# Optimization experiments

Measured on AMD Instinct MI355X. Metric: run time of the kernel, lower is better.

The kernel has to match this reference:

```python
import jax, jax.numpy as jnp
import numpy as np

B, N, H, R = 128, 512, 256, 3
VIRTUAL_DECAY = 0.7


def _build_tree():
    # Deterministic random recursive tree: parent[i] ~ U[0, i)
    rng = np.random.default_rng(0)
    parent = np.zeros(N, np.int64)
    for i in range(1, N):
        parent[i] = rng.integers(0, i)
    depth = np.zeros(N, np.int64)
    for i in range(1, N):
        depth[i] = depth[parent[i]] + 1
    rel_edge = rng.integers(0, R, N)          # relation type of edge (parent -> i)
    virtual = rng.random(N) < 0.1
    children = [[] for _ in range(N)]
    for i in range(1, N):
        children[parent[i]].append(i)
    # Group internal nodes by depth (deepest first == valid post-order batching),
    # pad ragged child lists per level.
    levels = []
    for d in range(int(depth.max()), -1, -1):
        nodes = [n for n in range(N) if depth[n] == d and len(children[n]) > 0]
        if not nodes:
            continue
        cmax = max(len(children[n]) for n in nodes)
        M = len(nodes)
        cidx = np.zeros((M, cmax), np.int64)
        cmask = np.zeros((M, cmax), np.float32)
        crel = np.zeros((M, cmax), np.int64)
        cvirt = np.zeros((M, cmax), bool)
        for m, n in enumerate(nodes):
            ch = children[n]
            k = len(ch)
            cidx[m, :k] = ch
            cmask[m, :k] = 1.0
            crel[m, :k] = rel_edge[ch]
            cvirt[m, :k] = virtual[ch]
        levels.append((jnp.array(nodes), jnp.array(cidx), jnp.array(cmask),
                       jnp.array(crel), jnp.array(cvirt)))
    return levels

LEVELS = _build_tree()


def _forward(node_features, W_enc, b_enc, rel_emb, W_i, b_i, W_o, b_o, W_u, b_u,
             W_f, b_f, w_attn, b_attn):
    h = node_features @ W_enc + b_enc            # (B, N, H) node_encoder
    c = jnp.zeros_like(h)
    for node_ids, cidx, cmask, crel, cvirt in LEVELS:
        x = h[:, node_ids]                       # (B, M, H) input_vec (== encoded feats)
        ch_h = h[:, cidx]                        # (B, M, C, H)
        ch_c = c[:, cidx]
        # virtual-node decay + padding mask
        decay = jnp.where(cvirt, VIRTUAL_DECAY, 1.0).astype(h.dtype) * cmask  # (M, C)
        ch_h = ch_h * decay[None, :, :, None]
        ch_c = ch_c * decay[None, :, :, None]
        # relation-aware attention over children
        re = rel_emb[crel]                       # (M, C, H)
        scores = jnp.einsum('bmch,h->bmc', re[None] + ch_h, w_attn) + b_attn[0]
        scores = jnp.where(cmask[None] > 0, scores, -1e9)
        attw = jax.nn.softmax(scores, axis=-1)   # (B, M, C)
        h_sum = jnp.einsum('bmc,bmch->bmh', attw, ch_h)
        # per-relation forget transform (note: original applies NO sigmoid here)
        f = jnp.zeros_like(ch_h)
        for r in range(R):
            fr = jnp.einsum('bmch,hk->bmck', ch_h, W_f[r]) + b_f[r]
            f = f + fr * (crel == r).astype(h.dtype)[None, :, :, None]
        c_sum = jnp.sum(f * ch_c, axis=2)        # (B, M, H); padded ch_c is 0
        comb = jnp.concatenate([x, h_sum], axis=-1)  # (B, M, 2H)
        i_g = jax.nn.sigmoid(comb @ W_i + b_i)
        o_g = jax.nn.sigmoid(comb @ W_o + b_o)
        u_g = jnp.tanh(comb @ W_u + b_u)
        c_new = i_g * u_g + c_sum
        h_new = o_g * jnp.tanh(c_new)
        h = h.at[:, node_ids].set(h_new)
        c = c.at[:, node_ids].set(c_new)
    return h[:, 0]                               # pooling == 'root' (root = 0)


def setup_inputs() -> dict:
    key = jax.random.key(0)
    ks = jax.random.split(key, 8)
    s = 0.05
    f32 = jnp.float32
    return {
        'node_features': jax.random.normal(ks[0], (B, N, H), f32),
        'W_enc': jax.random.normal(ks[1], (H, H), f32) * s,
        'b_enc': jnp.full((H,), 0.1, f32),
        'rel_emb': jax.random.normal(ks[2], (R, H), f32) * s,
        'W_i': jax.random.normal(ks[3], (2 * H, H), f32) * s,
        'b_i': jnp.full((H,), 0.1, f32),
        'W_o': jax.random.normal(ks[4], (2 * H, H), f32) * s,
        'b_o': jnp.full((H,), 0.1, f32),
        'W_u': jax.random.normal(ks[5], (2 * H, H), f32) * s,
        'b_u': jnp.full((H,), 0.1, f32),
        'W_f': jax.random.normal(ks[6], (R, H, H), f32) * s,
        'b_f': jnp.full((R, H), 0.1, f32),
        'w_attn': jax.random.normal(ks[7], (H,), f32) * s,
        'b_attn': jnp.full((1,), 0.1, f32),
    }


def reference(node_features, W_enc, b_enc, rel_emb, W_i, b_i, W_o, b_o, W_u, b_u,
              W_f, b_f, w_attn, b_attn):
    return _forward(node_features, W_enc, b_enc, rel_emb, W_i, b_i, W_o, b_o,
                    W_u, b_u, W_f, b_f, w_attn, b_attn)
```

## Files before the change

### kernel.cpp

```cpp
#include <hip/hip_runtime.h>
#include <stdint.h>
#include <string.h>
#include <math.h>

#define NB 128
#define NN 512
#define NH 256
#define NR 3

typedef __attribute__((ext_vector_type(8))) short bh8;
typedef __attribute__((ext_vector_type(4))) float f32x4;

struct Pcg {
  __uint128_t state, inc;
  bool has32; uint32_t buf32;
};

static const __uint128_t PCG_MULT =
    (((__uint128_t)2549297995355413924ULL) << 64) | 4865540595714422341ULL;

static inline uint64_t pcg_next64(Pcg& s) {
  s.state = s.state * PCG_MULT + s.inc;
  uint64_t hi = (uint64_t)(s.state >> 64), lo = (uint64_t)s.state;
  uint64_t x = hi ^ lo;
  unsigned rot = (unsigned)(s.state >> 122) & 63u;
  return (x >> rot) | (x << ((64u - rot) & 63u));
}
static inline uint32_t pcg_next32(Pcg& s) {
  if (s.has32) { s.has32 = false; return s.buf32; }
  uint64_t n = pcg_next64(s);
  s.has32 = true; s.buf32 = (uint32_t)(n >> 32);
  return (uint32_t)n;
}
static inline uint64_t pcg_bounded(Pcg& s, uint64_t high) {
  uint64_t rng = high - 1;
  if (rng == 0) return 0;
  uint32_t rng_excl = (uint32_t)rng + 1u;
  uint64_t m = (uint64_t)pcg_next32(s) * (uint64_t)rng_excl;
  uint32_t leftover = (uint32_t)m;
  if (leftover < rng_excl) {
    uint32_t threshold = (uint32_t)((0xFFFFFFFFu - (uint32_t)rng) % rng_excl);
    while (leftover < threshold) {
      m = (uint64_t)pcg_next32(s) * (uint64_t)rng_excl;
      leftover = (uint32_t)m;
    }
  }
  return m >> 32;
}
static inline double pcg_double(Pcg& s) {
  return (double)(pcg_next64(s) >> 11) * (1.0 / 9007199254740992.0);
}

static void pcg_seed0(Pcg& s) {
  uint32_t pool[4];
  uint32_t hc = 0x43b0d7e5u;
  auto hashmix = [&hc](uint32_t v) -> uint32_t {
    v ^= hc; hc *= 0x931e8875u; v *= hc; v ^= v >> 16; return v;
  };
  auto mix = [](uint32_t x, uint32_t y) -> uint32_t {
    uint32_t r = 0xca01f9ddu * x - 0x4973f715u * y; r ^= r >> 16; return r;
  };
  for (int i = 0; i < 4; i++) pool[i] = hashmix(0u);
  for (int src = 0; src < 4; src++)
    for (int dst = 0; dst < 4; dst++)
      if (src != dst) pool[dst] = mix(pool[dst], hashmix(pool[src]));
  uint32_t gs[8]; uint32_t hb = 0x8b51f9ddu;
  for (int i = 0; i < 8; i++) {
    uint32_t dv = pool[i & 3];
    dv ^= hb; hb *= 0x58f38dedu; dv *= hb; dv ^= dv >> 16;
    gs[i] = dv;
  }
  uint64_t w0 = (uint64_t)gs[0] | ((uint64_t)gs[1] << 32);
  uint64_t w1 = (uint64_t)gs[2] | ((uint64_t)gs[3] << 32);
  uint64_t w2 = (uint64_t)gs[4] | ((uint64_t)gs[5] << 32);
  uint64_t w3 = (uint64_t)gs[6] | ((uint64_t)gs[7] << 32);
  __uint128_t initstate = (((__uint128_t)w0) << 64) | w1;
  __uint128_t initseq   = (((__uint128_t)w2) << 64) | w3;
  s.state = 0;
  s.inc = (initseq << 1) | 1;
  s.state = s.state * PCG_MULT + s.inc;
  s.state += initstate;
  s.state = s.state * PCG_MULT + s.inc;
  s.has32 = false; s.buf32 = 0;
}

struct TreeMeta {
  int nodes[512];
  int cstart[512];
  int ccount[512];
  int echild[512];
  int erel[512];
  float edecay[512];
  int cechild[512];
  int cerel[512];
  float cedec[512];
  int cens[513];
};
struct HostTree {
  TreeMeta meta;
  int n_levels;
  int level_off[520];
  int level_M[520];
};

static void build_tree_host(HostTree& T) {
  Pcg st; pcg_seed0(st);
  int parent[NN], depth[NN], rel[NN];
  unsigned char virt[NN];
  parent[0] = 0; depth[0] = 0;
  for (int i = 1; i < NN; i++) parent[i] = (int)pcg_bounded(st, (uint64_t)i);
  for (int i = 1; i < NN; i++) depth[i] = depth[parent[i]] + 1;
  for (int i = 0; i < NN; i++) rel[i] = (int)pcg_bounded(st, (uint64_t)NR);
  for (int i = 0; i < NN; i++) virt[i] = (pcg_double(st) < 0.1) ? 1 : 0;

  int childcnt[NN]; memset(childcnt, 0, sizeof(childcnt));
  for (int i = 1; i < NN; i++) childcnt[parent[i]]++;
  int maxd = 0;
  for (int i = 0; i < NN; i++) if (depth[i] > maxd) maxd = depth[i];

  int ni = 0, ne = 0, nec = 0;
  T.n_levels = 0;
  for (int d = maxd; d >= 0; d--) {
    int mstart = ni;
    for (int n = 0; n < NN; n++) {
      if (depth[n] == d && childcnt[n] > 0) {
        T.meta.nodes[ni] = n;
        T.meta.cstart[ni] = ne;
        T.meta.ccount[ni] = childcnt[n];
        T.meta.cens[ni] = nec;
        for (int i2 = 1; i2 < NN; i2++) {
          if (parent[i2] == n) {
            T.meta.echild[ne] = i2;
            T.meta.erel[ne] = rel[i2];
            T.meta.edecay[ne] = virt[i2] ? 0.7f : 1.0f;
            ne++;
            if (childcnt[i2] > 0) {
              T.meta.cechild[nec] = i2;
              T.meta.cerel[nec] = rel[i2];
              T.meta.cedec[nec] = virt[i2] ? 0.7f : 1.0f;
              nec++;
            }
          }
        }
        ni++;
      }
    }
    if (ni > mstart) {
      T.level_off[T.n_levels] = mstart;
      T.level_M[T.n_levels] = ni - mstart;
      T.n_levels++;
    }
  }
  T.meta.cens[ni] = nec;
}

__device__ __forceinline__ uint16_t f2bf(float f) {
  uint32_t u = __float_as_uint(f);
  return (uint16_t)((u + 0x7fffu + ((u >> 16) & 1u)) >> 16);
}
__device__ __forceinline__ float bf2f(uint16_t b) {
  return __uint_as_float(((uint32_t)b) << 16);
}
__device__ __forceinline__ float sigm(float x) {
  return 1.f / (1.f + expf(-x));
}

__device__ __forceinline__ void stage_bf16(uint16_t* __restrict__ sm,
    const uint16_t* __restrict__ src, int stride, int rows) {
  const int chunks = rows << 3;
  for (int cch = threadIdx.x; cch < chunks; cch += 256) {
    const int row = cch >> 3, k = (cch & 7) << 3;
    uint4 v = *(const uint4*)(src + (size_t)row * stride + k);
    *(uint4*)(sm + (((row << 6) + k) ^ ((row & 7) << 3))) = v;
  }
}
__device__ __forceinline__ void stage_f32(uint16_t* __restrict__ sm,
    const float* __restrict__ src, int stride, int rows) {
  const int chunks = rows << 3;
  for (int cch = threadIdx.x; cch < chunks; cch += 256) {
    const int row = cch >> 3, k = (cch & 7) << 3;
    const float* p = src + (size_t)row * stride + k;
    float4 a = *(const float4*)p, b = *(const float4*)(p + 4);
    uint4 w;
    w.x = (uint32_t)f2bf(a.x) | ((uint32_t)f2bf(a.y) << 16);
    w.y = (uint32_t)f2bf(a.z) | ((uint32_t)f2bf(a.w) << 16);
    w.z = (uint32_t)f2bf(b.x) | ((uint32_t)f2bf(b.y) << 16);
    w.w = (uint32_t)f2bf(b.z) | ((uint32_t)f2bf(b.w) << 16);
    *(uint4*)(sm + (((row << 6) + k) ^ ((row & 7) << 3))) = w;
  }
}
__device__ __forceinline__ bh8 fld(const uint16_t* __restrict__ sm, int row, int k) {
  return *(const bh8*)(sm + (((row << 6) + k) ^ ((row & 7) << 3)));
}

#define LDROW(BUF, CH) do { \
    const uint4* p_ = (const uint4*)(hbase + (size_t)(CH) * NH); \
    BUF[0]=p_[0]; BUF[1]=p_[1]; BUF[2]=p_[2]; BUF[3]=p_[3]; \
    BUF[4]=p_[4]; BUF[5]=p_[5]; BUF[6]=p_[6]; BUF[7]=p_[7]; } while (0)
#define ACCROW(BUF, W) do { const float w_ = (W); \
    _Pragma("unroll") for (int v_ = 0; v_ < 8; v_++) { \
      const uint16_t* pe_ = (const uint16_t*)&BUF[v_]; \
      _Pragma("unroll") for (int q_ = 0; q_ < 8; q_++) \
        hs[v_*8+q_] = fmaf(bf2f(pe_[q_]), w_, hs[v_*8+q_]); } } while (0)

__global__ __launch_bounds__(256) void k_prep(const float* __restrict__ We,
    const float* __restrict__ Wf, const float* __restrict__ Wi,
    const float* __restrict__ Wo, const float* __restrict__ Wu,
    uint16_t* __restrict__ WeT, uint16_t* __restrict__ WfT,
    uint16_t* __restrict__ WgT) {
  const int i = blockIdx.x * 256 + threadIdx.x;
  if (i < 65536) {
    const int n = i >> 8, k = i & 255;
    WeT[i] = f2bf(We[k * 256 + n]);
  }
  const int i2 = i - 65536;
  if (i2 >= 0 && i2 < 196608) {
    const int r = i2 >> 16, rem = i2 & 65535, n = rem >> 8, k = rem & 255;
    WfT[i2] = f2bf(Wf[r * 65536 + k * 256 + n]);
  }
  const int i3 = i - 262144;
  if (i3 >= 0 && i3 < 393216) {
    const int g = i3 >> 17, rem = i3 & 131071, n = rem >> 9, k = rem & 511;
    const float* S = (g == 0) ? Wi : (g == 1) ? Wo : Wu;
    WgT[i3] = f2bf(S[k * 256 + n]);
  }
}

__global__ __launch_bounds__(256) void k_enc(const float* __restrict__ nf,
    const uint16_t* __restrict__ WeT, const float* __restrict__ b_enc,
    uint16_t* __restrict__ h_bf, uint16_t* __restrict__ x_enc) {
  __shared__ __align__(16) uint16_t smA[128 * 64];
  __shared__ __align__(16) uint16_t smB[128 * 64];
  const int bm = blockIdx.x * 128, bn = blockIdx.y * 128;
  const int tid = threadIdx.x, wid = tid >> 6, lane = tid & 63;
  const int wr = wid >> 1, wc2 = wid & 1, lr = lane & 15, lk = (lane >> 4) << 3;
  f32x4 acc[4][4] = {};
  for (int k0 = 0; k0 < 256; k0 += 64) {
    __syncthreads();
    stage_f32(smA, nf + (size_t)bm * NH + k0, NH, 128);
    stage_bf16(smB, WeT + (size_t)bn * 256 + k0, 256, 128);
    __syncthreads();
#pragma unroll
    for (int ks = 0; ks < 2; ks++) {
      bh8 af[4], bfr[4];
#pragma unroll
      for (int i = 0; i < 4; i++) af[i] = fld(smA, wr * 64 + i * 16 + lr, ks * 32 + lk);
#pragma unroll
      for (int j = 0; j < 4; j++) bfr[j] = fld(smB, wc2 * 64 + j * 16 + lr, ks * 32 + lk);
#pragma unroll
      for (int i = 0; i < 4; i++)
#pragma unroll
        for (int j = 0; j < 4; j++)
          acc[i][j] = __builtin_amdgcn_mfma_f32_16x16x32_bf16(af[i], bfr[j], acc[i][j], 0, 0, 0);
    }
  }
#pragma unroll
  for (int i = 0; i < 4; i++) {
#pragma unroll
    for (int j = 0; j < 4; j++) {
      const int col = bn + wc2 * 64 + j * 16 + (lane & 15);
      const float be = b_enc[col];
#pragma unroll
      for (int r = 0; r < 4; r++) {
        const int row = bm + wr * 64 + i * 16 + (lane >> 4) * 4 + r;
        const uint16_t hv = f2bf(acc[i][j][r] + be);
        h_bf[(size_t)row * NH + col] = hv;
        x_enc[(size_t)row * NH + col] = hv;
      }
    }
  }
}

__global__ __launch_bounds__(256) void k_sv0(const uint16_t* __restrict__ h_bf,
    const float* __restrict__ w_attn, float* __restrict__ svp) {
  const int idx = blockIdx.x * 256 + threadIdx.x;
  const int g = idx & 15;
  const size_t row = (size_t)(idx >> 4);
  const uint16_t* hp = h_bf + row * NH + g * 16;
  uint4 p0 = *(const uint4*)hp, p1 = *(const uint4*)(hp + 8);
  const uint16_t* e0 = (const uint16_t*)&p0;
  const uint16_t* e1 = (const uint16_t*)&p1;
  float s = 0.f;
#pragma unroll
  for (int u = 0; u < 8; u++) s = fmaf(bf2f(e0[u]), w_attn[g * 16 + u], s);
#pragma unroll
  for (int u = 0; u < 8; u++) s = fmaf(bf2f(e1[u]), w_attn[g * 16 + 8 + u], s);
  svp[idx] = s;
}

__global__ __launch_bounds__(256) void k_tiny(
    uint16_t* h_bf, float* c, float* __restrict__ svp,
    const uint16_t* __restrict__ x_enc,
    const uint16_t* __restrict__ WfT, const uint16_t* __restrict__ WgT,
    const float* __restrict__ b_f, const float* __restrict__ b_i,
    const float* __restrict__ b_o, const float* __restrict__ b_u,
    const float* __restrict__ rel_emb, const float* __restrict__ w_attn,
    const float* __restrict__ b_attn, float* __restrict__ out,
    const TreeMeta* __restrict__ tm, int nb) {
  __shared__ float sc[64 * 65];
  __shared__ float swa[256];
  __shared__ float sRE[3];
  __shared__ int chl[64]; __shared__ int rll[64]; __shared__ float dcl[64];
  __shared__ __align__(16) uint16_t hsum[4 * 4096];

  const int c0 = blockIdx.x * 16;
  const int mloc = blockIdx.y >> 1, b0 = (blockIdx.y & 1) * 64;
  const int gi = nb + mloc;
  const int nd = tm->nodes[gi], cs = tm->cstart[gi], cc = tm->ccount[gi];
  const int ce0 = tm->cens[gi], nic = tm->cens[gi + 1] - ce0;
  const int tid = threadIdx.x, wid = tid >> 6, lane = tid & 63;
  const int lb = lane & 15, lq = lane >> 4;
  const int colw = c0 + lb;
  const int wrow = b0 + wid * 16;

  if (tid < cc) {
    chl[tid] = tm->echild[cs + tid];
    rll[tid] = tm->erel[cs + tid];
    dcl[tid] = tm->edecay[cs + tid];
  }
  swa[tid] = w_attn[tid];
  if (wid < 3) {
    float p = 0.f;
#pragma unroll
    for (int i = 0; i < 4; i++) p += rel_emb[wid * NH + lane + 64 * i] * w_attn[lane + 64 * i];
#pragma unroll
    for (int off = 32; off; off >>= 1) p += __shfl_down(p, off);
    if (lane == 0) sRE[wid] = p;
  }
  __syncthreads();

  const float ba = b_attn[0];
  if (tid < 64) {
    const float* svpb = svp + (size_t)(b0 + tid) * NN * 16;
    for (int e = 0; e < cc; e++) {
      const float4* p = (const float4*)(svpb + chl[e] * 16);
      float4 a = p[0], b2 = p[1], c2 = p[2], d2 = p[3];
      float s = ((a.x + a.y) + (a.z + a.w)) + ((b2.x + b2.y) + (b2.z + b2.w)) +
                ((c2.x + c2.y) + (c2.z + c2.w)) + ((d2.x + d2.y) + (d2.z + d2.w));
      sc[tid * 65 + e] = sRE[rll[e]] + dcl[e] * s + ba;
    }
    float mx = -1e30f;
    for (int e = 0; e < cc; e++) mx = fmaxf(mx, sc[tid * 65 + e]);
    float ss = 0.f;
    for (int e = 0; e < cc; e++) ss += expf(sc[tid * 65 + e] - mx);
    const float inv = 1.0f / ss;
    for (int e = 0; e < cc; e++) sc[tid * 65 + e] = expf(sc[tid * 65 + e] - mx) * inv * dcl[e];
  }
  __syncthreads();

  const int sb = tid >> 2, sq = tid & 3;
  {
    float hs[64];
#pragma unroll
    for (int v = 0; v < 64; v++) hs[v] = 0.f;
    const uint16_t* hbase = h_bf + (size_t)(b0 + sb) * NN * NH + sq * 64;
    uint4 bufA[8], bufB[8];
    LDROW(bufA, chl[0]);
    int e = 0;
    for (; e + 2 <= cc; e += 2) {
      LDROW(bufB, chl[e + 1]);
      ACCROW(bufA, sc[sb * 65 + e]);
      if (e + 2 < cc) LDROW(bufA, chl[e + 2]);
      ACCROW(bufB, sc[sb * 65 + e + 1]);
    }
    if (e < cc) ACCROW(bufA, sc[sb * 65 + e]);
    uint16_t* sub = hsum + sq * 4096;
#pragma unroll
    for (int v = 0; v < 32; v++) {
      uint32_t pk = (uint32_t)f2bf(hs[2 * v]) | ((uint32_t)f2bf(hs[2 * v + 1]) << 16);
      const int elem = ((sb << 6) + 2 * v) ^ ((sb & 7) << 3);
      *(uint32_t*)(sub + elem) = pk;
    }
  }

  f32x4 csum = {};
#pragma unroll 2
  for (int e = 0; e < nic; e++) {
    const int ch = tm->cechild[ce0 + e];
    const int rel = tm->cerel[ce0 + e];
    const float dec = tm->cedec[ce0 + e];
    const uint16_t* Wr = WfT + (size_t)rel * 65536 + (size_t)colw * 256;
    f32x4 facc = {};
#pragma unroll
    for (int k0 = 0; k0 < 8; k0++) {
      const int kk = k0 * 32 + lq * 8;
      const bh8 af = *(const bh8*)(h_bf + ((size_t)(wrow + lb) * NN + ch) * NH + kk);
      const bh8 bq = *(const bh8*)(Wr + kk);
      facc = __builtin_amdgcn_mfma_f32_16x16x32_bf16(af, bq, facc, 0, 0, 0);
    }
    const float bfv = b_f[rel * NH + colw];
#pragma unroll
    for (int r = 0; r < 4; r++) {
      const int brow = wrow + lq * 4 + r;
      const float cch = c[((size_t)brow * NN + ch) * NH + colw];
      csum[r] += (dec * facc[r] + bfv) * (dec * cch);
    }
  }
  __syncthreads();

  f32x4 ga[3] = {};
#pragma unroll
  for (int k32 = 0; k32 < 16; k32++) {
    const int kk = k32 * 32 + lq * 8;
    bh8 af;
    if (k32 < 8) {
      af = *(const bh8*)(x_enc + ((size_t)(wrow + lb) * NN + nd) * NH + kk);
    } else {
      const int kx = k32 - 8;
      af = fld(hsum + (kx >> 1) * 4096, wid * 16 + lb, (kx & 1) * 32 + lq * 8);
    }
#pragma unroll
    for (int g = 0; g < 3; g++) {
      const bh8 bq = *(const bh8*)(WgT + ((size_t)g << 17) + (size_t)colw * 512 + kk);
      ga[g] = __builtin_amdgcn_mfma_f32_16x16x32_bf16(af, bq, ga[g], 0, 0, 0);
    }
  }

  const float bi_ = b_i[colw], bo_ = b_o[colw], bu_ = b_u[colw];
  const float wac = swa[colw];
#pragma unroll
  for (int r = 0; r < 4; r++) {
    const int brow = wrow + lq * 4 + r;
    const size_t idx = ((size_t)brow * NN + nd) * NH + colw;
    const float ig = sigm(ga[0][r] + bi_);
    const float og = sigm(ga[1][r] + bo_);
    const float ug = tanhf(ga[2][r] + bu_);
    const float cn = fmaf(ig, ug, csum[r]);
    c[idx] = cn;
    const float hn = og * tanhf(cn);
    h_bf[idx] = f2bf(hn);
    if (nd == 0) out[(size_t)brow * NH + colw] = hn;
    float pv = hn * wac;
    pv += __shfl_xor(pv, 1); pv += __shfl_xor(pv, 2);
    pv += __shfl_xor(pv, 4); pv += __shfl_xor(pv, 8);
    if (lb == 0) svp[((size_t)brow * NN + nd) * 16 + (c0 >> 4)] = pv;
  }
}

extern "C" void kernel_launch(void* const* d_in, const int* in_sizes, int n_in,
                              void* d_out, int out_size, void* d_ws, size_t ws_size,
                              hipStream_t stream) {
  (void)in_sizes; (void)n_in; (void)out_size; (void)ws_size;
  const float* nf      = (const float*)d_in[0];
  const float* W_enc   = (const float*)d_in[1];
  const float* b_enc   = (const float*)d_in[2];
  const float* rel_emb = (const float*)d_in[3];
  const float* W_i     = (const float*)d_in[4];
  const float* b_i     = (const float*)d_in[5];
  const float* W_o     = (const float*)d_in[6];
  const float* b_o     = (const float*)d_in[7];
  const float* W_u     = (const float*)d_in[8];
  const float* b_u     = (const float*)d_in[9];
  const float* W_f     = (const float*)d_in[10];
  const float* b_f     = (const float*)d_in[11];
  const float* w_attn  = (const float*)d_in[12];
  const float* b_attn  = (const float*)d_in[13];
  float* out = (float*)d_out;

  static HostTree T;
  build_tree_host(T);

  char* ws = (char*)d_ws;
  const size_t OFF_HBF = 32768;
  const size_t SZ_HBF  = (size_t)NB * NN * NH * 2;
  const size_t OFF_XE  = OFF_HBF + SZ_HBF;
  const size_t OFF_WET = OFF_XE + SZ_HBF;
  const size_t OFF_WFT = OFF_WET + 131072;
  const size_t OFF_WGT = OFF_WFT + 393216;
  const size_t OFF_C   = OFF_WGT + 786432;
  const size_t SZ_C    = (size_t)NB * NN * NH * 4;
  const size_t OFF_SVP = OFF_C + SZ_C;

  TreeMeta* dm = (TreeMeta*)ws;
  uint16_t* h_bf = (uint16_t*)(ws + OFF_HBF);
  uint16_t* x_enc = (uint16_t*)(ws + OFF_XE);
  uint16_t* WeT = (uint16_t*)(ws + OFF_WET);
  uint16_t* WfT = (uint16_t*)(ws + OFF_WFT);
  uint16_t* WgT = (uint16_t*)(ws + OFF_WGT);
  float* c = (float*)(ws + OFF_C);
  float* svp = (float*)(ws + OFF_SVP);

  hipMemcpyAsync(dm, &T.meta, sizeof(TreeMeta), hipMemcpyHostToDevice, stream);

  k_prep<<<2560, 256, 0, stream>>>(W_enc, W_f, W_i, W_o, W_u, WeT, WfT, WgT);
  k_enc<<<dim3((NB * NN) / 128, 2), 256, 0, stream>>>(nf, WeT, b_enc, h_bf, x_enc);
  k_sv0<<<dim3((NB * NN * 16) / 256), 256, 0, stream>>>(h_bf, w_attn, svp);

  for (int l = 0; l < T.n_levels; l++) {
    k_tiny<<<dim3(16, 2 * T.level_M[l]), 256, 0, stream>>>(h_bf, c, svp, x_enc,
        WfT, WgT, b_f, b_i, b_o, b_u, rel_emb, w_attn, b_attn, out, dm,
        T.level_off[l]);
  }
}
```

Measured before the change: 653.6 us.

## Split per-level tree LSTM kernel into attention/forget-cell and gate kernels

The fused per-level kernel is split in two. The first kernel does the attention-weighted child hidden sum, written to a global comb buffer, and the forget-gate cell contributions, which run in separate blocks per internal child edge and use atomicAdd into the parent's pre-zeroed c. The second kernel runs the gate GEMM with 64x64 tiles per block over x_enc and comb, which gives better register reuse of weights. This exposes more parallelism and removes the single block's serial loop over children. In exchange it adds a full memset of c, float atomics, an extra launch per level chunk, and a global round trip for comb.

```diff
diff --git a/kernel.cpp b/kernel.cpp
--- a/kernel.cpp
+++ b/kernel.cpp
@@ -92,6 +92,7 @@
   int erel[512];
   float edecay[512];
   int cechild[512];
+  int cepar[512];
   int cerel[512];
   float cedec[512];
   int cens[513];
@@ -136,6 +137,7 @@
             ne++;
             if (childcnt[i2] > 0) {
               T.meta.cechild[nec] = i2;
+              T.meta.cepar[nec] = n;
               T.meta.cerel[nec] = rel[i2];
               T.meta.cedec[nec] = virt[i2] ? 0.7f : 1.0f;
               nec++;
@@ -288,68 +290,92 @@
   svp[idx] = s;
 }
 
-__global__ __launch_bounds__(256) void k_tiny(
-    uint16_t* h_bf, float* c, float* __restrict__ svp,
-    const uint16_t* __restrict__ x_enc,
-    const uint16_t* __restrict__ WfT, const uint16_t* __restrict__ WgT,
-    const float* __restrict__ b_f, const float* __restrict__ b_i,
-    const float* __restrict__ b_o, const float* __restrict__ b_u,
+__global__ __launch_bounds__(256) void k_ac(
+    const uint16_t* __restrict__ h_bf, float* c, const float* __restrict__ svp,
+    const uint16_t* __restrict__ WfT, const float* __restrict__ b_f,
     const float* __restrict__ rel_emb, const float* __restrict__ w_attn,
-    const float* __restrict__ b_attn, float* __restrict__ out,
-    const TreeMeta* __restrict__ tm, int nb) {
-  __shared__ float sc[64 * 65];
-  __shared__ float swa[256];
-  __shared__ float sRE[3];
-  __shared__ int chl[64]; __shared__ int rll[64]; __shared__ float dcl[64];
-  __shared__ __align__(16) uint16_t hsum[4 * 4096];
-
-  const int c0 = blockIdx.x * 16;
-  const int mloc = blockIdx.y >> 1, b0 = (blockIdx.y & 1) * 64;
-  const int gi = nb + mloc;
-  const int nd = tm->nodes[gi], cs = tm->cstart[gi], cc = tm->ccount[gi];
-  const int ce0 = tm->cens[gi], nic = tm->cens[gi + 1] - ce0;
+    const float* __restrict__ b_attn, uint16_t* __restrict__ comb,
+    const TreeMeta* __restrict__ tm, int nb, int M, int ce0) {
   const int tid = threadIdx.x, wid = tid >> 6, lane = tid & 63;
-  const int lb = lane & 15, lq = lane >> 4;
-  const int colw = c0 + lb;
-  const int wrow = b0 + wid * 16;
-
-  if (tid < cc) {
-    chl[tid] = tm->echild[cs + tid];
-    rll[tid] = tm->erel[cs + tid];
-    dcl[tid] = tm->edecay[cs + tid];
-  }
-  swa[tid] = w_attn[tid];
-  if (wid < 3) {
-    float p = 0.f;
-#pragma unroll
-    for (int i = 0; i < 4; i++) p += rel_emb[wid * NH + lane + 64 * i] * w_attn[lane + 64 * i];
-#pragma unroll
-    for (int off = 32; off; off >>= 1) p += __shfl_down(p, off);
-    if (lane == 0) sRE[wid] = p;
-  }
-  __syncthreads();
-
-  const float ba = b_attn[0];
-  if (tid < 64) {
-    const float* svpb = svp + (size_t)(b0 + tid) * NN * 16;
-    for (int e = 0; e < cc; e++) {
-      const float4* p = (const float4*)(svpb + chl[e] * 16);
-      float4 a = p[0], b2 = p[1], c2 = p[2], d2 = p[3];
-      float s = ((a.x + a.y) + (a.z + a.w)) + ((b2.x + b2.y) + (b2.z + b2.w)) +
-                ((c2.x + c2.y) + (c2.z + c2.w)) + ((d2.x + d2.y) + (d2.z + d2.w));
-      sc[tid * 65 + e] = sRE[rll[e]] + dcl[e] * s + ba;
-    }
-    float mx = -1e30f;
-    for (int e = 0; e < cc; e++) mx = fmaxf(mx, sc[tid * 65 + e]);
-    float ss = 0.f;
-    for (int e = 0; e < cc; e++) ss += expf(sc[tid * 65 + e] - mx);
-    const float inv = 1.0f / ss;
-    for (int e = 0; e < cc; e++) sc[tid * 65 + e] = expf(sc[tid * 65 + e] - mx) * inv * dcl[e];
-  }
-  __syncthreads();
-
-  const int sb = tid >> 2, sq = tid & 3;
-  {
+  const int bx = blockIdx.x;
+
+  if (bx >= 2 * M) {
+    const int e8 = bx - 2 * M;
+    const int ce = ce0 + (e8 >> 3);
+    const int sub = e8 & 7;
+    const int b0 = (sub >> 2) * 64, cslice = (sub & 3) * 64;
+    const int ch = tm->cechild[ce], par = tm->cepar[ce], rel = tm->cerel[ce];
+    const float dec = tm->cedec[ce];
+    const int lr2 = lane & 15, hi4 = lane >> 4, lk = hi4 << 3;
+    const int colw = cslice + wid * 16 + lr2;
+    const uint16_t* Wr = WfT + (size_t)rel * 65536 + (size_t)colw * 256;
+    f32x4 facc[4] = {};
+#pragma unroll
+    for (int k0 = 0; k0 < 8; k0++) {
+      const int kk = k0 * 32 + lk;
+      bh8 af[4];
+#pragma unroll
+      for (int i = 0; i < 4; i++)
+        af[i] = *(const bh8*)(h_bf + ((size_t)(b0 + i * 16 + lr2) * NN + ch) * NH + kk);
+      const bh8 bq = *(const bh8*)(Wr + kk);
+#pragma unroll
+      for (int i = 0; i < 4; i++)
+        facc[i] = __builtin_amdgcn_mfma_f32_16x16x32_bf16(af[i], bq, facc[i], 0, 0, 0);
+    }
+    const float bfv = b_f[rel * NH + colw];
+#pragma unroll
+    for (int i = 0; i < 4; i++) {
+#pragma unroll
+      for (int r = 0; r < 4; r++) {
+        const int brow = b0 + i * 16 + hi4 * 4 + r;
+        const float cch = c[((size_t)brow * NN + ch) * NH + colw];
+        atomicAdd(&c[((size_t)brow * NN + par) * NH + colw],
+                  (dec * facc[i][r] + bfv) * (dec * cch));
+      }
+    }
+  } else {
+    __shared__ float sc[64 * 65];
+    __shared__ float sRE[3];
+    __shared__ int chl[64]; __shared__ int rll[64]; __shared__ float dcl[64];
+    const int mloc = bx >> 1, b0 = (bx & 1) * 64;
+    const int gi = nb + mloc;
+    const int cs = tm->cstart[gi], cc = tm->ccount[gi];
+
+    if (tid < cc) {
+      chl[tid] = tm->echild[cs + tid];
+      rll[tid] = tm->erel[cs + tid];
+      dcl[tid] = tm->edecay[cs + tid];
+    }
+    if (wid < 3) {
+      float p = 0.f;
+#pragma unroll
+      for (int i = 0; i < 4; i++) p += rel_emb[wid * NH + lane + 64 * i] * w_attn[lane + 64 * i];
+#pragma unroll
+      for (int off = 32; off; off >>= 1) p += __shfl_down(p, off);
+      if (lane == 0) sRE[wid] = p;
+    }
+    __syncthreads();
+
+    const float ba = b_attn[0];
+    if (tid < 64) {
+      const float* svpb = svp + (size_t)(b0 + tid) * NN * 16;
+      for (int e = 0; e < cc; e++) {
+        const float4* p = (const float4*)(svpb + chl[e] * 16);
+        float4 a = p[0], b2 = p[1], c2 = p[2], d2 = p[3];
+        float s = ((a.x + a.y) + (a.z + a.w)) + ((b2.x + b2.y) + (b2.z + b2.w)) +
+                  ((c2.x + c2.y) + (c2.z + c2.w)) + ((d2.x + d2.y) + (d2.z + d2.w));
+        sc[tid * 65 + e] = sRE[rll[e]] + dcl[e] * s + ba;
+      }
+      float mx = -1e30f;
+      for (int e = 0; e < cc; e++) mx = fmaxf(mx, sc[tid * 65 + e]);
+      float ss = 0.f;
+      for (int e = 0; e < cc; e++) ss += expf(sc[tid * 65 + e] - mx);
+      const float inv = 1.0f / ss;
+      for (int e = 0; e < cc; e++) sc[tid * 65 + e] = expf(sc[tid * 65 + e] - mx) * inv * dcl[e];
+    }
+    __syncthreads();
+
+    const int sb = tid >> 2, sq = tid & 3;
     float hs[64];
 #pragma unroll
     for (int v = 0; v < 64; v++) hs[v] = 0.f;
@@ -364,76 +390,79 @@
       ACCROW(bufB, sc[sb * 65 + e + 1]);
     }
     if (e < cc) ACCROW(bufA, sc[sb * 65 + e]);
-    uint16_t* sub = hsum + sq * 4096;
-#pragma unroll
-    for (int v = 0; v < 32; v++) {
-      uint32_t pk = (uint32_t)f2bf(hs[2 * v]) | ((uint32_t)f2bf(hs[2 * v + 1]) << 16);
-      const int elem = ((sb << 6) + 2 * v) ^ ((sb & 7) << 3);
-      *(uint32_t*)(sub + elem) = pk;
-    }
-  }
-
-  f32x4 csum = {};
-#pragma unroll 2
-  for (int e = 0; e < nic; e++) {
-    const int ch = tm->cechild[ce0 + e];
-    const int rel = tm->cerel[ce0 + e];
-    const float dec = tm->cedec[ce0 + e];
-    const uint16_t* Wr = WfT + (size_t)rel * 65536 + (size_t)colw * 256;
-    f32x4 facc = {};
-#pragma unroll
-    for (int k0 = 0; k0 < 8; k0++) {
-      const int kk = k0 * 32 + lq * 8;
-      const bh8 af = *(const bh8*)(h_bf + ((size_t)(wrow + lb) * NN + ch) * NH + kk);
-      const bh8 bq = *(const bh8*)(Wr + kk);
-      facc = __builtin_amdgcn_mfma_f32_16x16x32_bf16(af, bq, facc, 0, 0, 0);
-    }
-    const float bfv = b_f[rel * NH + colw];
+    uint16_t* cb = comb + ((size_t)(mloc * 128 + b0 + sb)) * 256 + sq * 64;
+#pragma unroll
+    for (int v = 0; v < 8; v++) {
+      uint4 w;
+      w.x = (uint32_t)f2bf(hs[8 * v + 0]) | ((uint32_t)f2bf(hs[8 * v + 1]) << 16);
+      w.y = (uint32_t)f2bf(hs[8 * v + 2]) | ((uint32_t)f2bf(hs[8 * v + 3]) << 16);
+      w.z = (uint32_t)f2bf(hs[8 * v + 4]) | ((uint32_t)f2bf(hs[8 * v + 5]) << 16);
+      w.w = (uint32_t)f2bf(hs[8 * v + 6]) | ((uint32_t)f2bf(hs[8 * v + 7]) << 16);
+      *(uint4*)(cb + v * 8) = w;
+    }
+  }
+}
+
+__global__ __launch_bounds__(256) void k_gates(
+    uint16_t* h_bf, float* c, float* __restrict__ svp,
+    const uint16_t* __restrict__ x_enc, const uint16_t* __restrict__ comb,
+    const uint16_t* __restrict__ WgT,
+    const float* __restrict__ b_i, const float* __restrict__ b_o,
+    const float* __restrict__ b_u, const float* __restrict__ w_attn,
+    float* __restrict__ out, const TreeMeta* __restrict__ tm, int nb) {
+  const int bx = blockIdx.x, mloc = bx >> 1, b0 = (bx & 1) * 64;
+  const int cslice = blockIdx.y * 64;
+  const int gi = nb + mloc;
+  const int nd = tm->nodes[gi];
+  const int tid = threadIdx.x, wid = tid >> 6, lane = tid & 63;
+  const int lr2 = lane & 15, hi4 = lane >> 4, lk = hi4 << 3;
+  const int colw = cslice + wid * 16 + lr2;
+
+  f32x4 ga[3][4] = {};
+#pragma unroll
+  for (int k32 = 0; k32 < 16; k32++) {
+    const int kk = k32 * 32 + lk;
+    bh8 af[4], bq[3];
+    if (k32 < 8) {
+#pragma unroll
+      for (int i = 0; i < 4; i++)
+        af[i] = *(const bh8*)(x_enc + ((size_t)(b0 + i * 16 + lr2) * NN + nd) * NH + kk);
+    } else {
+#pragma unroll
+      for (int i = 0; i < 4; i++)
+        af[i] = *(const bh8*)(comb + ((size_t)(mloc * 128 + b0 + i * 16 + lr2)) * 256 + (kk - 256));
+    }
+#pragma unroll
+    for (int g = 0; g < 3; g++)
+      bq[g] = *(const bh8*)(WgT + ((size_t)g << 17) + (size_t)colw * 512 + kk);
+#pragma unroll
+    for (int g = 0; g < 3; g++)
+#pragma unroll
+      for (int i = 0; i < 4; i++)
+        ga[g][i] = __builtin_amdgcn_mfma_f32_16x16x32_bf16(af[i], bq[g], ga[g][i], 0, 0, 0);
+  }
+
+  const float bi_ = b_i[colw], bo_ = b_o[colw], bu_ = b_u[colw];
+  const float wac = w_attn[colw];
+#pragma unroll
+  for (int i = 0; i < 4; i++) {
 #pragma unroll
     for (int r = 0; r < 4; r++) {
-      const int brow = wrow + lq * 4 + r;
-      const float cch = c[((size_t)brow * NN + ch) * NH + colw];
-      csum[r] += (dec * facc[r] + bfv) * (dec * cch);
-    }
-  }
-  __syncthreads();
-
-  f32x4 ga[3] = {};
-#pragma unroll
-  for (int k32 = 0; k32 < 16; k32++) {
-    const int kk = k32 * 32 + lq * 8;
-    bh8 af;
-    if (k32 < 8) {
-      af = *(const bh8*)(x_enc + ((size_t)(wrow + lb) * NN + nd) * NH + kk);
-    } else {
-      const int kx = k32 - 8;
-      af = fld(hsum + (kx >> 1) * 4096, wid * 16 + lb, (kx & 1) * 32 + lq * 8);
-    }
-#pragma unroll
-    for (int g = 0; g < 3; g++) {
-      const bh8 bq = *(const bh8*)(WgT + ((size_t)g << 17) + (size_t)colw * 512 + kk);
-      ga[g] = __builtin_amdgcn_mfma_f32_16x16x32_bf16(af, bq, ga[g], 0, 0, 0);
-    }
-  }
-
-  const float bi_ = b_i[colw], bo_ = b_o[colw], bu_ = b_u[colw];
-  const float wac = swa[colw];
-#pragma unroll
-  for (int r = 0; r < 4; r++) {
-    const int brow = wrow + lq * 4 + r;
-    const size_t idx = ((size_t)brow * NN + nd) * NH + colw;
-    const float ig = sigm(ga[0][r] + bi_);
-    const float og = sigm(ga[1][r] + bo_);
-    const float ug = tanhf(ga[2][r] + bu_);
-    const float cn = fmaf(ig, ug, csum[r]);
-    c[idx] = cn;
-    const float hn = og * tanhf(cn);
-    h_bf[idx] = f2bf(hn);
-    if (nd == 0) out[(size_t)brow * NH + colw] = hn;
-    float pv = hn * wac;
-    pv += __shfl_xor(pv, 1); pv += __shfl_xor(pv, 2);
-    pv += __shfl_xor(pv, 4); pv += __shfl_xor(pv, 8);
-    if (lb == 0) svp[((size_t)brow * NN + nd) * 16 + (c0 >> 4)] = pv;
+      const int brow = b0 + i * 16 + hi4 * 4 + r;
+      const size_t idx = ((size_t)brow * NN + nd) * NH + colw;
+      const float ig = sigm(ga[0][i][r] + bi_);
+      const float og = sigm(ga[1][i][r] + bo_);
+      const float ug = tanhf(ga[2][i][r] + bu_);
+      const float cn = fmaf(ig, ug, c[idx]);
+      c[idx] = cn;
+      const float hn = og * tanhf(cn);
+      h_bf[idx] = f2bf(hn);
+      if (nd == 0) out[(size_t)brow * NH + colw] = hn;
+      float pv = hn * wac;
+      pv += __shfl_xor(pv, 1); pv += __shfl_xor(pv, 2);
+      pv += __shfl_xor(pv, 4); pv += __shfl_xor(pv, 8);
+      if (lr2 == 0) svp[((size_t)brow * NN + nd) * 16 + (cslice >> 4) + wid] = pv;
+    }
   }
 }
 
@@ -461,15 +490,16 @@
   build_tree_host(T);
 
   char* ws = (char*)d_ws;
-  const size_t OFF_HBF = 32768;
-  const size_t SZ_HBF  = (size_t)NB * NN * NH * 2;
-  const size_t OFF_XE  = OFF_HBF + SZ_HBF;
-  const size_t OFF_WET = OFF_XE + SZ_HBF;
-  const size_t OFF_WFT = OFF_WET + 131072;
-  const size_t OFF_WGT = OFF_WFT + 393216;
-  const size_t OFF_C   = OFF_WGT + 786432;
-  const size_t SZ_C    = (size_t)NB * NN * NH * 4;
-  const size_t OFF_SVP = OFF_C + SZ_C;
+  const size_t OFF_HBF  = 32768;
+  const size_t SZ_HBF   = (size_t)NB * NN * NH * 2;
+  const size_t OFF_XE   = OFF_HBF + SZ_HBF;
+  const size_t OFF_WET  = OFF_XE + SZ_HBF;
+  const size_t OFF_WFT  = OFF_WET + 131072;
+  const size_t OFF_WGT  = OFF_WFT + 393216;
+  const size_t OFF_C    = OFF_WGT + 786432;
+  const size_t SZ_C     = (size_t)NB * NN * NH * 4;
+  const size_t OFF_SVP  = OFF_C + SZ_C;
+  const size_t OFF_COMB = OFF_SVP + (size_t)NB * NN * 16 * 4;
 
   TreeMeta* dm = (TreeMeta*)ws;
   uint16_t* h_bf = (uint16_t*)(ws + OFF_HBF);
@@ -479,16 +509,26 @@
   uint16_t* WgT = (uint16_t*)(ws + OFF_WGT);
   float* c = (float*)(ws + OFF_C);
   float* svp = (float*)(ws + OFF_SVP);
+  uint16_t* comb = (uint16_t*)(ws + OFF_COMB);
 
   hipMemcpyAsync(dm, &T.meta, sizeof(TreeMeta), hipMemcpyHostToDevice, stream);
+  hipMemsetAsync(c, 0, SZ_C, stream);
 
   k_prep<<<2560, 256, 0, stream>>>(W_enc, W_f, W_i, W_o, W_u, WeT, WfT, WgT);
   k_enc<<<dim3((NB * NN) / 128, 2), 256, 0, stream>>>(nf, WeT, b_enc, h_bf, x_enc);
   k_sv0<<<dim3((NB * NN * 16) / 256), 256, 0, stream>>>(h_bf, w_attn, svp);
 
   for (int l = 0; l < T.n_levels; l++) {
-    k_tiny<<<dim3(16, 2 * T.level_M[l]), 256, 0, stream>>>(h_bf, c, svp, x_enc,
-        WfT, WgT, b_f, b_i, b_o, b_u, rel_emb, w_attn, b_attn, out, dm,
-        T.level_off[l]);
-  }
-}
+    const int Mfull = T.level_M[l];
+    for (int c0 = 0; c0 < Mfull; c0 += 128) {
+      const int Mc = (Mfull - c0) < 128 ? (Mfull - c0) : 128;
+      const int nb = T.level_off[l] + c0;
+      const int ce0 = T.meta.cens[nb];
+      const int nCE = T.meta.cens[nb + Mc] - ce0;
+      k_ac<<<dim3(2 * Mc + 8 * nCE), 256, 0, stream>>>(h_bf, c, svp, WfT, b_f,
+          rel_emb, w_attn, b_attn, comb, dm, nb, Mc, ce0);
+      k_gates<<<dim3(2 * Mc, 4), 256, 0, stream>>>(h_bf, c, svp, x_enc, comb,
+          WgT, b_i, b_o, b_u, w_attn, out, dm, nb);
+    }
+  }
+}
```

Measured after the change: 692.7 us. +6.0%, slower.
